# Kernel optimization log

Hardware: AMD Instinct MI355X
Metric: run time of the kernel (lower is better)

Reference implementation:

```python
import jax, jax.numpy as jnp
import numpy as np

B, S, D, E = 8, 4096, 2048, 8
CHUNK = 128
TAU = 0.7


def setup_inputs() -> dict:
    key = jax.random.key(0)
    k0, k1, k2 = jax.random.split(key, 3)
    H = D // 2
    x = jax.random.normal(k0, (B, S, D), dtype=jnp.float32)
    W1 = jax.random.normal(k1, (D, H), dtype=jnp.float32) * (1.0 / np.sqrt(D))
    b1 = jnp.zeros((H,), dtype=jnp.float32)
    W2 = jax.random.normal(k2, (H, E), dtype=jnp.float32) * (1.0 / np.sqrt(H))
    b2 = jnp.zeros((E,), dtype=jnp.float32)
    return {"x": x, "W1": W1, "b1": b1, "W2": W2, "b2": b2}


def reference(x, W1, b1, W2, b2):
    b, s, d = x.shape
    e = W2.shape[1]
    c = s // CHUNK  # num_chunks (seq_len divisible by chunk_size)
    # router MLP: Linear -> ReLU -> Linear
    logits = jnp.maximum(x @ W1 + b1, 0.0) @ W2 + b2  # [B,S,E]
    # per-chunk mean logits
    chunk_logits = logits.reshape(b, c, CHUNK, e).mean(axis=2)  # [B,C,E]
    bidx = jnp.arange(b)
    # chunk 0: plain argmax
    init = jnp.argmax(chunk_logits[:, 0], axis=-1)  # [B]
    # chunks 1..C-1: hysteresis recurrence via scan
    def step(prev, cl):  # cl: [B,E]
        ce = jnp.argmax(cl, axis=-1)
        diff = cl[bidx, ce] - cl[bidx, prev]
        new = jnp.where(diff > TAU, ce, prev)
        return new, new
    _, rest = jax.lax.scan(step, init, jnp.swapaxes(chunk_logits[:, 1:], 0, 1))
    expert_indices = jnp.concatenate([init[:, None], rest.T], axis=1)  # [B,C]
    oh = jax.nn.one_hot(expert_indices, e, dtype=logits.dtype)  # [B,C,E]
    routing_weights = jnp.broadcast_to(oh[:, :, None, :], (b, c, CHUNK, e)).reshape(b, s, e)
    return routing_weights, expert_indices
```

## Files before the change

### kernel.cpp

```cpp
#include <hip/hip_runtime.h>

typedef unsigned int uint;
typedef unsigned short ushort;

#define BB 8
#define SS 4096
#define DD 2048
#define HH 1024
#define EE 8
#define CHUNK 128
#define NCHUNK 32
#define TAU 0.7f

#define BM 128
#define BN 256
#define BK 32
#define KITERS (DD / BK)
#define NSLICE (HH / BN)

typedef short bf16x8 __attribute__((ext_vector_type(8)));
typedef float f32x16 __attribute__((ext_vector_type(16)));

__device__ inline uint pack_rn(float a, float b) {
    uint ua = __float_as_uint(a), ub = __float_as_uint(b);
    ua += 0x7FFFu + ((ua >> 16) & 1u);
    ub += 0x7FFFu + ((ub >> 16) & 1u);
    return (ua >> 16) | (ub & 0xFFFF0000u);
}

__global__ __launch_bounds__(256) void reorder_w1_kernel(
    const float* __restrict__ W1, ushort* __restrict__ w1b)
{
    const int kg = blockIdx.x >> 2;
    const int n  = ((blockIdx.x & 3) << 8) + threadIdx.x;
    float v[8];
#pragma unroll
    for (int j = 0; j < 8; ++j) v[j] = W1[(size_t)(kg * 8 + j) * HH + n];
    uint pk[4];
#pragma unroll
    for (int p = 0; p < 4; ++p) pk[p] = pack_rn(v[2 * p], v[2 * p + 1]);
    const size_t off = (size_t)kg * HH + n;
    ((uint4*)w1b)[off] = make_uint4(pk[0], pk[1], pk[2], pk[3]);
}

__global__ __launch_bounds__(256, 2) void router_gemm_kernel(
    const float* __restrict__ x,
    const ushort* __restrict__ w1b,
    const float* __restrict__ b1,
    const float* __restrict__ W2,
    float* __restrict__ chunk_logits)
{
    const int slice = blockIdx.x;
    const int bc    = blockIdx.y;
    const int n0    = slice * BN;

    const int tid  = threadIdx.x;
    const int wave = tid >> 6;
    const int lane = tid & 63;
    const int lm   = lane & 31;
    const int kq   = lane >> 5;
    const int wn   = wave * 64;

    __shared__ __align__(16) ushort As[4][BM][8];
    __shared__ __align__(16) ushort Bs[4][BN][8];
    __shared__ float  W2s[BN][EE];
    __shared__ float  b1s[BN];
    __shared__ float  red[4][EE];

    const float* xrow = x + (size_t)bc * CHUNK * DD;

    ((float4*)&W2s[0][0])[tid]       = ((const float4*)(W2 + (size_t)n0 * EE))[tid];
    ((float4*)&W2s[0][0])[tid + 256] = ((const float4*)(W2 + (size_t)n0 * EE))[tid + 256];
    if (tid < BN / 4) ((float4*)b1s)[tid] = ((const float4*)(b1 + n0))[tid];

    f32x16 acc[4][2];
#pragma unroll
    for (int i = 0; i < 4; ++i)
#pragma unroll
        for (int j = 0; j < 2; ++j)
#pragma unroll
            for (int r = 0; r < 16; ++r) acc[i][j][r] = 0.0f;

    const int am = tid >> 1;
    const int ah = tid & 1;

    for (int it = 0; it < KITERS; ++it) {
        const int k0 = it * BK;
        __syncthreads();

        {
            const int kgg = (k0 >> 3) + wave;
#pragma unroll
            for (int h = 0; h < 4; ++h) {
                const size_t goff = ((size_t)kgg * HH + n0 + h * 64 + lane) * 8;
                __builtin_amdgcn_global_load_lds(
                    (const __attribute__((address_space(1))) uint*)(w1b + goff),
                    (__attribute__((address_space(3))) uint*)&Bs[wave][h * 64 + lane][0],
                    16, 0, 0);
            }
        }

        {
            const float* src = xrow + (size_t)am * DD + k0 + ah * 16;
            float4 v0 = ((const float4*)src)[0];
            float4 v1 = ((const float4*)src)[1];
            float4 v2 = ((const float4*)src)[2];
            float4 v3 = ((const float4*)src)[3];
            const float f[16] = {v0.x, v0.y, v0.z, v0.w, v1.x, v1.y, v1.z, v1.w,
                                 v2.x, v2.y, v2.z, v2.w, v3.x, v3.y, v3.z, v3.w};
            uint pk[8];
#pragma unroll
            for (int p = 0; p < 8; ++p) pk[p] = pack_rn(f[2 * p], f[2 * p + 1]);
            const int kg0 = ah * 2;
            *(uint4*)&As[kg0][am][0]     = make_uint4(pk[0], pk[1], pk[2], pk[3]);
            *(uint4*)&As[kg0 + 1][am][0] = make_uint4(pk[4], pk[5], pk[6], pk[7]);
        }

        __syncthreads();

#pragma unroll
        for (int s = 0; s < 2; ++s) {
            const int kg = 2 * s + kq;
            bf16x8 a[4], b[2];
#pragma unroll
            for (int i = 0; i < 4; ++i)
                a[i] = *(const bf16x8*)&As[kg][i * 32 + lm][0];
#pragma unroll
            for (int j = 0; j < 2; ++j)
                b[j] = *(const bf16x8*)&Bs[kg][wn + j * 32 + lm][0];
#pragma unroll
            for (int i = 0; i < 4; ++i)
#pragma unroll
                for (int j = 0; j < 2; ++j)
                    acc[i][j] = __builtin_amdgcn_mfma_f32_32x32x16_bf16(
                        a[i], b[j], acc[i][j], 0, 0, 0);
        }
    }

    float part[EE];
#pragma unroll
    for (int e = 0; e < EE; ++e) part[e] = 0.0f;

#pragma unroll
    for (int j = 0; j < 2; ++j) {
        const int hl = wn + j * 32 + lm;
        const float bias = b1s[hl];
        float w2r[EE];
#pragma unroll
        for (int e = 0; e < EE; ++e) w2r[e] = W2s[hl][e];
#pragma unroll
        for (int i = 0; i < 4; ++i)
#pragma unroll
            for (int r = 0; r < 16; ++r) {
                const float hv = fmaxf(acc[i][j][r] + bias, 0.0f);
#pragma unroll
                for (int e = 0; e < EE; ++e) part[e] = fmaf(hv, w2r[e], part[e]);
            }
    }

#pragma unroll
    for (int off = 32; off >= 1; off >>= 1)
#pragma unroll
        for (int e = 0; e < EE; ++e) part[e] += __shfl_down(part[e], off, 64);

    if (lane == 0)
#pragma unroll
        for (int e = 0; e < EE; ++e) red[wave][e] = part[e];
    __syncthreads();
    if (tid < EE) {
        const float s = red[0][tid] + red[1][tid] + red[2][tid] + red[3][tid];
        atomicAdd(&chunk_logits[(size_t)bc * EE + tid], s * (1.0f / CHUNK));
    }
}

__global__ void hysteresis_kernel(const float* __restrict__ chunk_logits,
                                  const float* __restrict__ b2,
                                  int* __restrict__ eidx_ws,
                                  float* __restrict__ out_idx)
{
    __shared__ float cls[BB * NCHUNK * EE];
    const int tid = threadIdx.x;
#pragma unroll
    for (int i = 0; i < 8; ++i)
        ((float4*)cls)[tid + i * 64] = ((const float4*)chunk_logits)[tid + i * 64];
    __syncthreads();

    const int b = tid;
    if (b >= BB) return;
    float b2r[EE];
#pragma unroll
    for (int e = 0; e < EE; ++e) b2r[e] = b2[e];

    const float* cl = cls + b * NCHUNK * EE;
    int prev = 0;
    for (int c = 0; c < NCHUNK; ++c) {
        float v[EE];
        float best = -3.4e38f;
        int ce = 0;
#pragma unroll
        for (int e = 0; e < EE; ++e) {
            const float lv = cl[c * EE + e] + b2r[e];
            v[e] = lv;
            if (lv > best) { best = lv; ce = e; }
        }
        if (c == 0) prev = ce;
        else if (best - v[prev] > TAU) prev = ce;
        eidx_ws[b * NCHUNK + c] = prev;
        out_idx[b * NCHUNK + c] = (float)prev;
    }
}

__global__ __launch_bounds__(256) void onehot_kernel(const int* __restrict__ eidx,
                                                     float* __restrict__ out)
{
    const int tok = blockIdx.x * blockDim.x + threadIdx.x;
    if (tok >= BB * SS) return;
    const int b = tok / SS;
    const int s = tok - b * SS;
    const int idx = eidx[b * NCHUNK + (s / CHUNK)];
    float vals[EE];
#pragma unroll
    for (int e = 0; e < EE; ++e) vals[e] = (e == idx) ? 1.0f : 0.0f;
    float4* o = (float4*)(out + (size_t)tok * EE);
    o[0] = make_float4(vals[0], vals[1], vals[2], vals[3]);
    o[1] = make_float4(vals[4], vals[5], vals[6], vals[7]);
}

extern "C" void kernel_launch(void* const* d_in, const int* in_sizes, int n_in,
                              void* d_out, int out_size, void* d_ws, size_t ws_size,
                              hipStream_t stream)
{
    const float* x  = (const float*)d_in[0];
    const float* W1 = (const float*)d_in[1];
    const float* b1 = (const float*)d_in[2];
    const float* W2 = (const float*)d_in[3];
    const float* b2 = (const float*)d_in[4];
    float* out = (float*)d_out;

    ushort* w1b          = (ushort*)d_ws;
    float*  chunk_logits = (float*)((char*)d_ws + (size_t)8 * 1024 * 1024);
    int*    eidx         = (int*)((char*)d_ws + (size_t)8 * 1024 * 1024 + 8192);

    hipMemsetAsync(chunk_logits, 0, BB * NCHUNK * EE * sizeof(float), stream);

    reorder_w1_kernel<<<1024, 256, 0, stream>>>(W1, w1b);

    dim3 grid(NSLICE, BB * NCHUNK);
    router_gemm_kernel<<<grid, 256, 0, stream>>>(x, w1b, b1, W2, chunk_logits);

    hysteresis_kernel<<<1, 64, 0, stream>>>(chunk_logits, b2, eidx,
                                            out + (size_t)BB * SS * EE);

    onehot_kernel<<<(BB * SS + 255) / 256, 256, 0, stream>>>(eidx, out);
}
```

Before: 569.1 us.

## Double-buffer GEMM with async x loads, XCD-aware block mapping, fuse finalize kernels

The router GEMM now double-buffers LDS and prefetches both x (raw fp32 through global_load_lds) and W1 tiles for the next K step while MFMAs run on the current one. The x-to-bf16 conversion moves from the store path to the LDS-read path. Blocks are remapped so all four N slices of a chunk land on the same XCD, which should improve L2 reuse of x. The hysteresis and one-hot kernels are merged into one per-batch kernel to save a launch, at the cost of rerunning the serial recurrence in every block. The fp32 A tile doubles LDS use, which may lower occupancy.

```diff
diff --git a/kernel.cpp b/kernel.cpp
--- a/kernel.cpp
+++ b/kernel.cpp
@@ -50,8 +50,11 @@
     const float* __restrict__ W2,
     float* __restrict__ chunk_logits)
 {
-    const int slice = blockIdx.x;
-    const int bc    = blockIdx.y;
+    const int bid   = blockIdx.x;
+    const int xcd   = bid & 7;
+    const int loc   = bid >> 3;
+    const int bc    = xcd * 32 + (loc >> 2);
+    const int slice = loc & 3;
     const int n0    = slice * BN;
 
     const int tid  = threadIdx.x;
@@ -61,8 +64,8 @@
     const int kq   = lane >> 5;
     const int wn   = wave * 64;
 
-    __shared__ __align__(16) ushort As[4][BM][8];
-    __shared__ __align__(16) ushort Bs[4][BN][8];
+    __shared__ __align__(16) float  As_f[2][4][2][BM][4];
+    __shared__ __align__(16) ushort Bs[2][4][BN][8];
     __shared__ float  W2s[BN][EE];
     __shared__ float  b1s[BN];
     __shared__ float  red[4][EE];
@@ -81,61 +84,78 @@
 #pragma unroll
             for (int r = 0; r < 16; ++r) acc[i][j][r] = 0.0f;
 
-    const int am = tid >> 1;
-    const int ah = tid & 1;
-
-    for (int it = 0; it < KITERS; ++it) {
-        const int k0 = it * BK;
-        __syncthreads();
-
-        {
-            const int kgg = (k0 >> 3) + wave;
-#pragma unroll
-            for (int h = 0; h < 4; ++h) {
-                const size_t goff = ((size_t)kgg * HH + n0 + h * 64 + lane) * 8;
-                __builtin_amdgcn_global_load_lds(
-                    (const __attribute__((address_space(1))) uint*)(w1b + goff),
-                    (__attribute__((address_space(3))) uint*)&Bs[wave][h * 64 + lane][0],
-                    16, 0, 0);
-            }
-        }
-
-        {
-            const float* src = xrow + (size_t)am * DD + k0 + ah * 16;
-            float4 v0 = ((const float4*)src)[0];
-            float4 v1 = ((const float4*)src)[1];
-            float4 v2 = ((const float4*)src)[2];
-            float4 v3 = ((const float4*)src)[3];
-            const float f[16] = {v0.x, v0.y, v0.z, v0.w, v1.x, v1.y, v1.z, v1.w,
-                                 v2.x, v2.y, v2.z, v2.w, v3.x, v3.y, v3.z, v3.w};
-            uint pk[8];
-#pragma unroll
-            for (int p = 0; p < 8; ++p) pk[p] = pack_rn(f[2 * p], f[2 * p + 1]);
-            const int kg0 = ah * 2;
-            *(uint4*)&As[kg0][am][0]     = make_uint4(pk[0], pk[1], pk[2], pk[3]);
-            *(uint4*)&As[kg0 + 1][am][0] = make_uint4(pk[4], pk[5], pk[6], pk[7]);
-        }
-
-        __syncthreads();
-
-#pragma unroll
-        for (int s = 0; s < 2; ++s) {
-            const int kg = 2 * s + kq;
-            bf16x8 a[4], b[2];
-#pragma unroll
-            for (int i = 0; i < 4; ++i)
-                a[i] = *(const bf16x8*)&As[kg][i * 32 + lm][0];
-#pragma unroll
-            for (int j = 0; j < 2; ++j)
-                b[j] = *(const bf16x8*)&Bs[kg][wn + j * 32 + lm][0];
-#pragma unroll
-            for (int i = 0; i < 4; ++i)
-#pragma unroll
-                for (int j = 0; j < 2; ++j)
-                    acc[i][j] = __builtin_amdgcn_mfma_f32_32x32x16_bf16(
-                        a[i], b[j], acc[i][j], 0, 0, 0);
-        }
-    }
+#define STAGE(tp, buf) do {                                                          \
+        _Pragma("unroll")                                                            \
+        for (int i = 0; i < 4; ++i) {                                               \
+            const int half_ = i >> 1;                                                \
+            const int mrow_ = (i & 1) * 64 + lane;                                   \
+            const float* gsrc_ = xrow + (size_t)mrow_ * DD                           \
+                                 + ((tp) * BK + wave * 8 + half_ * 4);               \
+            __builtin_amdgcn_global_load_lds(                                        \
+                (const __attribute__((address_space(1))) uint*)gsrc_,                \
+                (__attribute__((address_space(3))) uint*)&As_f[buf][wave][half_][mrow_][0], \
+                16, 0, 0);                                                           \
+        }                                                                            \
+        {                                                                            \
+            const int kgg_ = (tp) * 4 + wave;                                        \
+            _Pragma("unroll")                                                        \
+            for (int h = 0; h < 4; ++h) {                                            \
+                const size_t goff_ = ((size_t)kgg_ * HH + n0 + h * 64 + lane) * 8;   \
+                __builtin_amdgcn_global_load_lds(                                    \
+                    (const __attribute__((address_space(1))) uint*)(w1b + goff_),    \
+                    (__attribute__((address_space(3))) uint*)&Bs[buf][wave][h * 64 + lane][0], \
+                    16, 0, 0);                                                       \
+            }                                                                        \
+        }                                                                            \
+    } while (0)
+
+#define MFMA_PHASE(buf) do {                                                         \
+        _Pragma("unroll")                                                            \
+        for (int s = 0; s < 2; ++s) {                                                \
+            const int kg = 2 * s + kq;                                               \
+            bf16x8 a[4], b[2];                                                       \
+            _Pragma("unroll")                                                        \
+            for (int i = 0; i < 4; ++i) {                                            \
+                const float4 lo = *(const float4*)&As_f[buf][kg][0][i * 32 + lm][0]; \
+                const float4 hi = *(const float4*)&As_f[buf][kg][1][i * 32 + lm][0]; \
+                uint4 pk4 = make_uint4(pack_rn(lo.x, lo.y), pack_rn(lo.z, lo.w),     \
+                                       pack_rn(hi.x, hi.y), pack_rn(hi.z, hi.w));    \
+                a[i] = *(bf16x8*)&pk4;                                               \
+            }                                                                        \
+            _Pragma("unroll")                                                        \
+            for (int j = 0; j < 2; ++j)                                              \
+                b[j] = *(const bf16x8*)&Bs[buf][kg][wn + j * 32 + lm][0];            \
+            __builtin_amdgcn_s_setprio(1);                                           \
+            _Pragma("unroll")                                                        \
+            for (int i = 0; i < 4; ++i)                                              \
+                _Pragma("unroll")                                                    \
+                for (int j = 0; j < 2; ++j)                                          \
+                    acc[i][j] = __builtin_amdgcn_mfma_f32_32x32x16_bf16(             \
+                        a[i], b[j], acc[i][j], 0, 0, 0);                             \
+            __builtin_amdgcn_s_setprio(0);                                           \
+        }                                                                            \
+    } while (0)
+
+    STAGE(0, 0);
+    asm volatile("s_waitcnt vmcnt(0)" ::: "memory");
+    __builtin_amdgcn_s_barrier();
+    asm volatile("" ::: "memory");
+
+    for (int t = 0; t < KITERS - 1; ++t) {
+        const int cur = t & 1;
+        STAGE(t + 1, cur ^ 1);
+        asm volatile("s_waitcnt vmcnt(8)" ::: "memory");
+        __builtin_amdgcn_s_barrier();
+        asm volatile("" ::: "memory");
+        MFMA_PHASE(cur);
+        asm volatile("s_waitcnt lgkmcnt(0)" ::: "memory");
+        __builtin_amdgcn_s_barrier();
+        asm volatile("" ::: "memory");
+    }
+    asm volatile("s_waitcnt vmcnt(0)" ::: "memory");
+    __builtin_amdgcn_s_barrier();
+    asm volatile("" ::: "memory");
+    MFMA_PHASE((KITERS - 1) & 1);
 
     float part[EE];
 #pragma unroll
@@ -173,57 +193,51 @@
     }
 }
 
-__global__ void hysteresis_kernel(const float* __restrict__ chunk_logits,
-                                  const float* __restrict__ b2,
-                                  int* __restrict__ eidx_ws,
-                                  float* __restrict__ out_idx)
-{
-    __shared__ float cls[BB * NCHUNK * EE];
+__global__ __launch_bounds__(256) void finalize_kernel(
+    const float* __restrict__ chunk_logits,
+    const float* __restrict__ b2,
+    float* __restrict__ out)
+{
+    __shared__ float cls[NCHUNK][EE];
+    __shared__ int   idxs[NCHUNK];
     const int tid = threadIdx.x;
-#pragma unroll
-    for (int i = 0; i < 8; ++i)
-        ((float4*)cls)[tid + i * 64] = ((const float4*)chunk_logits)[tid + i * 64];
+    const int b   = blockIdx.x >> 4;
+    const int sg  = blockIdx.x & 15;
+
+    {
+        const int c = tid >> 3, e = tid & 7;
+        cls[c][e] = chunk_logits[(size_t)(b * NCHUNK + c) * EE + e] + b2[e];
+    }
     __syncthreads();
 
-    const int b = tid;
-    if (b >= BB) return;
-    float b2r[EE];
-#pragma unroll
-    for (int e = 0; e < EE; ++e) b2r[e] = b2[e];
-
-    const float* cl = cls + b * NCHUNK * EE;
-    int prev = 0;
-    for (int c = 0; c < NCHUNK; ++c) {
-        float v[EE];
-        float best = -3.4e38f;
-        int ce = 0;
-#pragma unroll
-        for (int e = 0; e < EE; ++e) {
-            const float lv = cl[c * EE + e] + b2r[e];
-            v[e] = lv;
-            if (lv > best) { best = lv; ce = e; }
+    if (tid == 0) {
+        int prev = 0;
+        for (int c = 0; c < NCHUNK; ++c) {
+            float best = -3.4e38f;
+            int ce = 0;
+#pragma unroll
+            for (int e = 0; e < EE; ++e) {
+                const float lv = cls[c][e];
+                if (lv > best) { best = lv; ce = e; }
+            }
+            if (c == 0) prev = ce;
+            else if (best - cls[c][prev] > TAU) prev = ce;
+            idxs[c] = prev;
         }
-        if (c == 0) prev = ce;
-        else if (best - v[prev] > TAU) prev = ce;
-        eidx_ws[b * NCHUNK + c] = prev;
-        out_idx[b * NCHUNK + c] = (float)prev;
-    }
-}
-
-__global__ __launch_bounds__(256) void onehot_kernel(const int* __restrict__ eidx,
-                                                     float* __restrict__ out)
-{
-    const int tok = blockIdx.x * blockDim.x + threadIdx.x;
-    if (tok >= BB * SS) return;
-    const int b = tok / SS;
-    const int s = tok - b * SS;
-    const int idx = eidx[b * NCHUNK + (s / CHUNK)];
-    float vals[EE];
-#pragma unroll
-    for (int e = 0; e < EE; ++e) vals[e] = (e == idx) ? 1.0f : 0.0f;
-    float4* o = (float4*)(out + (size_t)tok * EE);
-    o[0] = make_float4(vals[0], vals[1], vals[2], vals[3]);
-    o[1] = make_float4(vals[4], vals[5], vals[6], vals[7]);
+    }
+    __syncthreads();
+
+    const int tok = sg * 256 + tid;
+    const int id  = idxs[tok >> 7];
+    float v[EE];
+#pragma unroll
+    for (int e = 0; e < EE; ++e) v[e] = (e == id) ? 1.0f : 0.0f;
+    float4* o = (float4*)(out + ((size_t)b * SS + tok) * EE);
+    o[0] = make_float4(v[0], v[1], v[2], v[3]);
+    o[1] = make_float4(v[4], v[5], v[6], v[7]);
+
+    if (sg == 0 && tid < NCHUNK)
+        out[(size_t)BB * SS * EE + b * NCHUNK + tid] = (float)idxs[tid];
 }
 
 extern "C" void kernel_launch(void* const* d_in, const int* in_sizes, int n_in,
@@ -239,17 +253,13 @@
 
     ushort* w1b          = (ushort*)d_ws;
     float*  chunk_logits = (float*)((char*)d_ws + (size_t)8 * 1024 * 1024);
-    int*    eidx         = (int*)((char*)d_ws + (size_t)8 * 1024 * 1024 + 8192);
 
     hipMemsetAsync(chunk_logits, 0, BB * NCHUNK * EE * sizeof(float), stream);
 
     reorder_w1_kernel<<<1024, 256, 0, stream>>>(W1, w1b);
 
-    dim3 grid(NSLICE, BB * NCHUNK);
-    router_gemm_kernel<<<grid, 256, 0, stream>>>(x, w1b, b1, W2, chunk_logits);
-
-    hysteresis_kernel<<<1, 64, 0, stream>>>(chunk_logits, b2, eidx,
-                                            out + (size_t)BB * SS * EE);
-
-    onehot_kernel<<<(BB * SS + 255) / 256, 256, 0, stream>>>(eidx, out);
-}
+    router_gemm_kernel<<<NSLICE * BB * NCHUNK, 256, 0, stream>>>(
+        x, w1b, b1, W2, chunk_logits);
+
+    finalize_kernel<<<BB * 16, 256, 0, stream>>>(chunk_logits, b2, out);
+}
```

After: 595.8 us. 1.05x slower.
